# Kernel optimization log

Hardware: AMD Instinct MI355X
Metric: run time of the kernel (lower is better)

The kernel has to match this reference:

```python
import jax, jax.numpy as jnp
import numpy as np

N = 100000
E = 6400000
D = 512


def setup_inputs() -> dict:
    key = jax.random.key(0)
    k1, k2, k3, k4 = jax.random.split(key, 4)
    x = jax.random.normal(k1, (N, D), dtype=jnp.float32)
    edge_index = jax.random.randint(k2, (2, E), 0, N, dtype=jnp.int64)
    edge_attr = jax.random.uniform(k3, (E,), dtype=jnp.float32)
    # xavier_normal_ on (in_feat, 1) with gain=1.414: std = gain*sqrt(2/(fan_in+fan_out))
    std = 1.414 * np.sqrt(2.0 / (D + 1))
    p = jax.random.normal(k4, (D, 1), dtype=jnp.float32) * std
    b = jnp.zeros((1,), dtype=jnp.float32)
    return {"x": x, "edge_index": edge_index, "edge_attr": edge_attr, "p": p, "b": b}


def reference(x, edge_index, edge_attr, p, b):
    # Per-node gate: sigmoid(x @ p + b), shape [N]
    diag_val = jax.nn.sigmoid(jnp.matmul(x, p) + b).reshape(-1)
    # spspmm(A, diag(d)) scales each edge value by d[col] = d[edge_index[1]]
    adj_mat_val = edge_attr * diag_val[edge_index[1]]
    return edge_index, adj_mat_val
```

## Files before the change

### kernel.cpp

```cpp
#include <hip/hip_runtime.h>
#include <math.h>


__global__ __launch_bounds__(256) void gate_kernel(
    const float* __restrict__ x,
    const float* __restrict__ p,
    const float* __restrict__ b,
    float* __restrict__ gate,
    int N)
{
    const int wave_id = (blockIdx.x * blockDim.x + threadIdx.x) >> 6;
    const int lane    = threadIdx.x & 63;
    const int nwaves  = (gridDim.x * blockDim.x) >> 6;
    const float bb = b[0];

    const float4* pr = (const float4*)p;
    float4 p0 = pr[lane * 2];
    float4 p1 = pr[lane * 2 + 1];

    for (int row = wave_id; row < N; row += nwaves) {
        const float4* xr = (const float4*)(x + (size_t)row * 512);
        float4 x0 = xr[lane * 2];
        float4 x1 = xr[lane * 2 + 1];
        float s = x0.x * p0.x + x0.y * p0.y + x0.z * p0.z + x0.w * p0.w
                + x1.x * p1.x + x1.y * p1.y + x1.z * p1.z + x1.w * p1.w;
        #pragma unroll
        for (int off = 32; off > 0; off >>= 1)
            s += __shfl_down(s, off, 64);
        if (lane == 0) {
            float t = s + bb;
            gate[row] = 1.0f / (1.0f + __expf(-t));
        }
    }
}

__global__ __launch_bounds__(256) void edge_kernel(
    const int*   __restrict__ edge_index,
    const float* __restrict__ edge_attr,
    const float* __restrict__ gate,
    float* __restrict__ out,
    int E)
{
    const int tid    = blockIdx.x * blockDim.x + threadIdx.x;
    const int stride = gridDim.x * blockDim.x;

    const int EI4 = (2 * E) >> 2;
    const int EV4 = E >> 2;

    const int4*  ei4  = (const int4*)edge_index;
    float4*      out4 = (float4*)out;
    for (int i = tid; i < EI4; i += stride) {
        int4 v = ei4[i];
        out4[i] = make_float4((float)v.x, (float)v.y, (float)v.z, (float)v.w);
    }

    const int4*   col4 = (const int4*)(edge_index + E);
    const float4* ea4  = (const float4*)edge_attr;
    float4*       ov4  = (float4*)(out + 2 * (size_t)E);
    for (int i = tid; i < EV4; i += stride) {
        int4   c = col4[i];
        float4 a = ea4[i];
        float4 r;
        r.x = a.x * gate[c.x];
        r.y = a.y * gate[c.y];
        r.z = a.z * gate[c.z];
        r.w = a.w * gate[c.w];
        ov4[i] = r;
    }
}

extern "C" void kernel_launch(void* const* d_in, const int* in_sizes, int n_in,
                              void* d_out, int out_size, void* d_ws, size_t ws_size,
                              hipStream_t stream) {
    const float* x          = (const float*)d_in[0];
    const int*   edge_index = (const int*)  d_in[1];
    const float* edge_attr  = (const float*)d_in[2];
    const float* p          = (const float*)d_in[3];
    const float* b          = (const float*)d_in[4];

    const int D = in_sizes[3];
    const int N = in_sizes[0] / D;
    const int E = in_sizes[2];

    float* gate = (float*)d_ws;
    float* out  = (float*)d_out;

    int gate_blocks = (N + 3) / 4;
    gate_kernel<<<gate_blocks, 256, 0, stream>>>(x, p, b, gate, N);

    int edge_blocks = ((2 * E / 4) + 255) / 256;
    edge_kernel<<<edge_blocks, 256, 0, stream>>>(edge_index, edge_attr, gate, out, E);
}
```

Before: 368.8 us.

## Fuse gate and edge kernels into one cooperative kernel with grid sync

Merges the gate computation and the edge scaling into one cooperative kernel on a fixed grid of 1024 blocks. The row-index conversion copy overlaps with the gate pass, and only the column copy and scaling wait behind a grid-wide barrier. Output stores become nontemporal to avoid polluting cache. This removes one launch and lets independent copy traffic run alongside the gate pass, but it depends on cooperative launch residency and adds the cost of a grid sync.

```diff
diff --git a/kernel.cpp b/kernel.cpp
--- a/kernel.cpp
+++ b/kernel.cpp
@@ -1,71 +1,80 @@
 #include <hip/hip_runtime.h>
+#include <hip/hip_cooperative_groups.h>
 #include <math.h>
 
+namespace cg = cooperative_groups;
 
-__global__ __launch_bounds__(256) void gate_kernel(
+
+typedef float fx4 __attribute__((ext_vector_type(4)));
+
+__global__ __launch_bounds__(256) void fused_kernel(
     const float* __restrict__ x,
     const float* __restrict__ p,
     const float* __restrict__ b,
-    float* __restrict__ gate,
-    int N)
+    const int*   __restrict__ edge_index,
+    const float* __restrict__ edge_attr,
+    float*       __restrict__ gate,
+    float*       __restrict__ out,
+    int N, int E)
 {
-    const int wave_id = (blockIdx.x * blockDim.x + threadIdx.x) >> 6;
-    const int lane    = threadIdx.x & 63;
-    const int nwaves  = (gridDim.x * blockDim.x) >> 6;
-    const float bb = b[0];
+    const int tid      = blockIdx.x * blockDim.x + threadIdx.x;
+    const int nthreads = gridDim.x * blockDim.x;
+    const int wave_id  = tid >> 6;
+    const int lane     = tid & 63;
+    const int nwaves   = nthreads >> 6;
 
-    const float4* pr = (const float4*)p;
-    float4 p0 = pr[lane * 2];
-    float4 p1 = pr[lane * 2 + 1];
-
-    for (int row = wave_id; row < N; row += nwaves) {
-        const float4* xr = (const float4*)(x + (size_t)row * 512);
-        float4 x0 = xr[lane * 2];
-        float4 x1 = xr[lane * 2 + 1];
-        float s = x0.x * p0.x + x0.y * p0.y + x0.z * p0.z + x0.w * p0.w
-                + x1.x * p1.x + x1.y * p1.y + x1.z * p1.z + x1.w * p1.w;
-        #pragma unroll
-        for (int off = 32; off > 0; off >>= 1)
-            s += __shfl_down(s, off, 64);
-        if (lane == 0) {
-            float t = s + bb;
-            gate[row] = 1.0f / (1.0f + __expf(-t));
+    {
+        const float bb = b[0];
+        const float4* pr = (const float4*)p;
+        const float4 p0 = pr[lane * 2];
+        const float4 p1 = pr[lane * 2 + 1];
+        for (int row = wave_id; row < N; row += nwaves) {
+            const float4* xr = (const float4*)(x + (size_t)row * 512);
+            float4 x0 = xr[lane * 2];
+            float4 x1 = xr[lane * 2 + 1];
+            float s = x0.x * p0.x + x0.y * p0.y + x0.z * p0.z + x0.w * p0.w
+                    + x1.x * p1.x + x1.y * p1.y + x1.z * p1.z + x1.w * p1.w;
+            #pragma unroll
+            for (int off = 32; off > 0; off >>= 1)
+                s += __shfl_down(s, off, 64);
+            if (lane == 0) {
+                float t = s + bb;
+                gate[row] = 1.0f / (1.0f + __expf(-t));
+            }
         }
     }
-}
 
-__global__ __launch_bounds__(256) void edge_kernel(
-    const int*   __restrict__ edge_index,
-    const float* __restrict__ edge_attr,
-    const float* __restrict__ gate,
-    float* __restrict__ out,
-    int E)
-{
-    const int tid    = blockIdx.x * blockDim.x + threadIdx.x;
-    const int stride = gridDim.x * blockDim.x;
-
-    const int EI4 = (2 * E) >> 2;
     const int EV4 = E >> 2;
 
-    const int4*  ei4  = (const int4*)edge_index;
-    float4*      out4 = (float4*)out;
-    for (int i = tid; i < EI4; i += stride) {
-        int4 v = ei4[i];
-        out4[i] = make_float4((float)v.x, (float)v.y, (float)v.z, (float)v.w);
+    {
+        const int4* row4 = (const int4*)edge_index;
+        fx4*        out4 = (fx4*)out;
+        for (int i = tid; i < EV4; i += nthreads) {
+            int4 v = row4[i];
+            fx4 f = { (float)v.x, (float)v.y, (float)v.z, (float)v.w };
+            __builtin_nontemporal_store(f, &out4[i]);
+        }
     }
 
-    const int4*   col4 = (const int4*)(edge_index + E);
-    const float4* ea4  = (const float4*)edge_attr;
-    float4*       ov4  = (float4*)(out + 2 * (size_t)E);
-    for (int i = tid; i < EV4; i += stride) {
-        int4   c = col4[i];
-        float4 a = ea4[i];
-        float4 r;
-        r.x = a.x * gate[c.x];
-        r.y = a.y * gate[c.y];
-        r.z = a.z * gate[c.z];
-        r.w = a.w * gate[c.w];
-        ov4[i] = r;
+    cg::this_grid().sync();
+
+    {
+        const int4*   col4 = (const int4*)(edge_index + E);
+        const float4* ea4  = (const float4*)edge_attr;
+        fx4*          outc = ((fx4*)out) + EV4;
+        fx4*          outv = (fx4*)(out + 2 * (size_t)E);
+        for (int i = tid; i < EV4; i += nthreads) {
+            int4   c = col4[i];
+            float4 a = ea4[i];
+            float g0 = gate[c.x];
+            float g1 = gate[c.y];
+            float g2 = gate[c.z];
+            float g3 = gate[c.w];
+            fx4 cf = { (float)c.x, (float)c.y, (float)c.z, (float)c.w };
+            __builtin_nontemporal_store(cf, &outc[i]);
+            fx4 r = { a.x * g0, a.y * g1, a.z * g2, a.w * g3 };
+            __builtin_nontemporal_store(r, &outv[i]);
+        }
     }
 }
 
@@ -79,15 +88,15 @@
     const float* b          = (const float*)d_in[4];
 
     const int D = in_sizes[3];
-    const int N = in_sizes[0] / D;
-    const int E = in_sizes[2];
+    int N = in_sizes[0] / D;
+    int E = in_sizes[2];
 
     float* gate = (float*)d_ws;
     float* out  = (float*)d_out;
 
-    int gate_blocks = (N + 3) / 4;
-    gate_kernel<<<gate_blocks, 256, 0, stream>>>(x, p, b, gate, N);
-
-    int edge_blocks = ((2 * E / 4) + 255) / 256;
-    edge_kernel<<<edge_blocks, 256, 0, stream>>>(edge_index, edge_attr, gate, out, E);
+    void* args[] = { (void*)&x, (void*)&p, (void*)&b, (void*)&edge_index,
+                     (void*)&edge_attr, (void*)&gate, (void*)&out,
+                     (void*)&N, (void*)&E };
+    (void)hipLaunchCooperativeKernel((void*)fused_kernel, dim3(1024), dim3(256),
+                                     args, 0, stream);
 }
```

Result: slower. 491.8 us (+33.4%).
